# Performance work log

Measured on AMD Instinct MI355X. Metric: run time of the kernel, lower is better.

## Reference

```python
import jax, jax.numpy as jnp
import numpy as np

# 3x3 Hessian/derivative stencils (match torch tensors in edge_mask_deptehwise)
_DII = jnp.array([[0., 1., 0.], [0., -2., 0.], [0., 1., 0.]], jnp.float32).reshape(1, 1, 3, 3)
_DIJ = 0.25 * jnp.array([[1., 0., -1.], [0., 0., 0.], [-1., 0., 1.]], jnp.float32).reshape(1, 1, 3, 3)
_DJJ = jnp.array([[0., 0., 0.], [1., -2., 1.], [0., 0., 0.]], jnp.float32).reshape(1, 1, 3, 3)


def _conv3x3(x, kern):  # x: [1,1,h,w], zero padding 1 (matches F.conv2d padding=1)
    return jax.lax.conv_general_dilated(x, kern, (1, 1), ((1, 1), (1, 1)))


def _edge_mask(x, edge_thld):  # x: [1,1,h,w] -> bool [1,1,h,w]
    dii = _conv3x3(x, _DII)
    dij = _conv3x3(x, _DIJ)
    djj = _conv3x3(x, _DJJ)
    det = dii * djj - dij * dij
    tr = dii + djj
    thld = (edge_thld + 1) ** 2 / edge_thld
    return (tr * tr / det <= thld) & (det > 0)


def _max_pool(x, ksize):  # stride 1, padding 1 (matches F.max_pool2d(..., padding=1))
    return jax.lax.reduce_window(x, -jnp.inf, jax.lax.max,
                                 (1, 1, ksize, ksize), (1, 1, 1, 1),
                                 ((0, 0), (0, 0), (1, 1), (1, 1)))


def setup_inputs() -> dict:
    key = jax.random.key(0)
    k1, k2 = jax.random.split(key)
    h = w = 4096
    score_map = jax.random.uniform(k1, (1, 1, h, w), dtype=jnp.float32)
    valid_depth_mask = jax.random.randint(k2, (h, w), 0, 2).astype(jnp.bool_)
    return {
        'score_map': score_map,
        'valid_depth_mask': valid_depth_mask,
        'k': 4096,
        'score_thld': 0,
        'edge_thld': 10,
        'nms_size': 3,
        'eof_size': 5,
    }


def reference(score_map, valid_depth_mask, k, score_thld, edge_thld, nms_size, eof_size):
    b, c, h, w = score_map.shape  # b = c = 1 (extract_kpts reshapes to (h, w))
    mask = score_map > score_thld
    if nms_size > 0:
        nms_max = _max_pool(score_map, nms_size)
        mask = (score_map == nms_max) & mask
    if eof_size > 0:
        ri = jnp.arange(h)
        cj = jnp.arange(w)
        eof = ((ri >= eof_size) & (ri < h - eof_size))[:, None] & \
              ((cj >= eof_size) & (cj < w - eof_size))[None, :]
        mask = eof[None, None] & mask
    if edge_thld > 0:
        mask = _edge_mask(score_map, edge_thld) & mask
    mask2d = mask.reshape(h, w) & valid_depth_mask
    flat_scores = score_map.reshape(h * w)
    # nonzero + argsort(desc)[:k] + gather  ==  top_k over -inf-masked scores
    masked = jnp.where(mask2d.reshape(-1), flat_scores, -jnp.inf)
    _, idx = jax.lax.top_k(masked, k)
    rows = idx // w
    cols = idx % w
    indices = jnp.stack([rows, cols], axis=0)[None]  # [1, 2, k]
    scores = flat_scores[idx][None]                  # [1, k]
    return indices, scores
```

## Files before the change

kernel.cpp:

```cpp
#include <hip/hip_runtime.h>
#include <stdint.h>

#define H 4096
#define W 4096
#define EOFS 5
#define K_TOP 4096
#define NB 65536
#define SLOT_CAP 8192
#define RPB 16
#define CBUF 4096
#define EMIT_LDS (K_TOP + 128)


__device__ __forceinline__ unsigned int bucket_of(float s) {
    float u = s * s;
    float u2 = u * u;
    float u4 = u2 * u2;
    float s9 = u4 * s;
    unsigned int b = (unsigned int)(s9 * 65536.0f);
    return b > 65535u ? 65535u : b;
}

__global__ void zero_kernel(unsigned int* hist, unsigned int* pivot,
                            unsigned int* candCount) {
    int p = blockIdx.x * blockDim.x + threadIdx.x;
    if (p < NB) hist[p] = 0u;
    if (p == 0) { pivot[0] = 0u; candCount[0] = 0u; }
}

#define PROC(ta, tb, tc, td, te, tf, tg, th, ti, jj)                           \
    {                                                                          \
        int j = (jj);                                                          \
        if (j >= EOFS && j <= W - 1 - EOFS) {                                  \
            float e = (te);                                                    \
            if (e > 0.0f) {                                                    \
                float m = fmaxf(fmaxf(fmaxf((ta), (tb)), fmaxf((tc), (td))),   \
                                fmaxf(fmaxf((tf), (tg)), fmaxf((th), (ti))));  \
                if (e >= m) {                                                  \
                    float dii = ((tb) - 2.0f * e) + (th);                      \
                    float djj = ((td) - 2.0f * e) + (tf);                      \
                    float dij = 0.25f * ((((ta) - (tc)) - (tg)) + (ti));       \
                    float det = dii * djj - dij * dij;                         \
                    if (det > 0.0f) {                                          \
                        float tr = dii + djj;                                  \
                        if (tr * tr / det <= 12.1f) {                          \
                            if (vmask[(size_t)i * W + j] != 0) {               \
                                unsigned int fb = __float_as_uint(e);          \
                                atomicAdd(&hist[bucket_of(e)], 1u);            \
                                unsigned int pos = atomicAdd(&cnt, 1u);        \
                                if (pos < CBUF) {                              \
                                    unsigned int idx =                         \
                                        (unsigned int)i * W + (unsigned int)j; \
                                    buf[pos] =                                 \
                                        ((unsigned long long)fb << 32) |       \
                                        (unsigned int)(~idx);                  \
                                }                                              \
                            }                                                  \
                        }                                                      \
                    }                                                          \
                }                                                              \
            }                                                                  \
        }                                                                      \
    }

__global__ __launch_bounds__(1024)
void collect_kernel(const float* __restrict__ x, const int* __restrict__ vmask,
                    unsigned int* __restrict__ hist,
                    unsigned long long* __restrict__ cand,
                    unsigned int* __restrict__ candCount,
                    unsigned int cand_cap, int do_cand) {
    __shared__ unsigned long long buf[CBUF];
    __shared__ unsigned int cnt, gbase;
    int t = threadIdx.x;
    if (t == 0) cnt = 0u;
    __syncthreads();
    int j0 = t * 4;
    bool active = (t >= 1 && t <= 1022);
    int r0 = EOFS + (int)blockIdx.x * RPB;
    int rend = r0 + RPB - 1;
    if (rend > H - 1 - EOFS) rend = H - 1 - EOFS;

    float al, a0, a1, a2, a3, ar;
    float bl, b0, b1, b2, b3, br;
    float cl, c0, c1, c2, c3, cr;
    if (active) {
        { const float* p = x + (size_t)(r0 - 1) * W + j0; al = p[-1];
          float4 q = *(const float4*)p; a0 = q.x; a1 = q.y; a2 = q.z; a3 = q.w; ar = p[4]; }
        { const float* p = x + (size_t)r0 * W + j0; bl = p[-1];
          float4 q = *(const float4*)p; b0 = q.x; b1 = q.y; b2 = q.z; b3 = q.w; br = p[4]; }
    }
    for (int i = r0; i <= rend; ++i) {
        if (active) {
            { const float* p = x + (size_t)(i + 1) * W + j0; cl = p[-1];
              float4 q = *(const float4*)p; c0 = q.x; c1 = q.y; c2 = q.z; c3 = q.w; cr = p[4]; }
            PROC(al, a0, a1, bl, b0, b1, cl, c0, c1, j0 + 0);
            PROC(a0, a1, a2, b0, b1, b2, c0, c1, c2, j0 + 1);
            PROC(a1, a2, a3, b1, b2, b3, c1, c2, c3, j0 + 2);
            PROC(a2, a3, ar, b2, b3, br, c2, c3, cr, j0 + 3);
            al = bl; a0 = b0; a1 = b1; a2 = b2; a3 = b3; ar = br;
            bl = cl; b0 = c0; b1 = c1; b2 = c2; b3 = c3; br = cr;
        }
    }
    __syncthreads();
    if (do_cand) {
        unsigned int c = cnt;
        if (c > CBUF) c = CBUF;
        if (t == 0) gbase = atomicAdd(candCount, c);
        __syncthreads();
        unsigned int g0 = gbase;
        for (unsigned int p = t; p < c; p += 1024)
            if (g0 + p < cand_cap) cand[g0 + p] = buf[p];
    }
}

__global__ __launch_bounds__(64)
void coarse_kernel(const unsigned int* __restrict__ hist,
                   unsigned int* __restrict__ coarse) {
    int c = blockIdx.x, t = threadIdx.x;
    const unsigned int* h = hist + c * 256;
    unsigned int s = h[t] + h[t + 64] + h[t + 128] + h[t + 192];
    for (int off = 32; off > 0; off >>= 1) s += __shfl_down(s, off, 64);
    if (t == 0) coarse[c] = s;
}

__global__ __launch_bounds__(256)
void chunkscan_kernel(const unsigned int* __restrict__ coarse,
                      unsigned int* __restrict__ chunkExcl) {
    __shared__ unsigned int s[256];
    int t = threadIdx.x;
    unsigned int mine = coarse[t];
    s[t] = mine;
    __syncthreads();
    for (int off = 1; off < 256; off <<= 1) {
        unsigned int v = (t + off < 256) ? s[t + off] : 0u;
        __syncthreads();
        s[t] += v;
        __syncthreads();
    }
    chunkExcl[t] = s[t] - mine;
}

__global__ __launch_bounds__(256)
void basefill_kernel(const unsigned int* __restrict__ hist,
                     const unsigned int* __restrict__ chunkExcl,
                     unsigned int* __restrict__ base,
                     unsigned int* __restrict__ pivotOut) {
    __shared__ unsigned int s[256];
    int t = threadIdx.x;
    int b = blockIdx.x * 256 + t;
    unsigned int h = hist[b];
    s[t] = h;
    __syncthreads();
    for (int off = 1; off < 256; off <<= 1) {
        unsigned int v = (t + off < 256) ? s[t + off] : 0u;
        __syncthreads();
        s[t] += v;
        __syncthreads();
    }
    unsigned int bb = chunkExcl[blockIdx.x] + s[t] - h;
    base[b] = bb;
    if (bb < (unsigned int)K_TOP && bb + h >= (unsigned int)K_TOP)
        pivotOut[0] = (unsigned int)b;
}

__global__ __launch_bounds__(256)
void scatter_cand_kernel(const unsigned long long* __restrict__ cand,
                         const unsigned int* __restrict__ candCount,
                         const unsigned int* __restrict__ pivotPtr,
                         unsigned int* __restrict__ base,
                         unsigned long long* __restrict__ slots,
                         unsigned int cand_cap) {
    unsigned int n = *candCount;
    if (n > cand_cap) n = cand_cap;
    unsigned int pivot = *pivotPtr;
    unsigned int stride = gridDim.x * blockDim.x;
    for (unsigned int p = blockIdx.x * blockDim.x + threadIdx.x; p < n; p += stride) {
        unsigned long long k = cand[p];
        unsigned int fb = (unsigned int)(k >> 32);
        unsigned int bkt = bucket_of(__uint_as_float(fb));
        if (bkt >= pivot) {
            unsigned int pos = atomicAdd(&base[bkt], 1u);
            if (pos < (unsigned int)SLOT_CAP) slots[pos] = k;
        }
    }
}

__global__ void scatter_full_kernel(const float* __restrict__ x,
                                    const int* __restrict__ vmask,
                                    const unsigned int* __restrict__ pivotPtr,
                                    unsigned int* __restrict__ base,
                                    unsigned long long* __restrict__ slots) {
    int j = EOFS + blockIdx.x * blockDim.x + threadIdx.x;
    int i = EOFS + blockIdx.y;
    if (j > W - 1 - EOFS) return;
    const float* r0p = x + (size_t)(i - 1) * W + j;
    const float* r1p = x + (size_t)i * W + j;
    const float* r2p = x + (size_t)(i + 1) * W + j;
    float a = r0p[-1], b = r0p[0], c = r0p[1];
    float d = r1p[-1], e = r1p[0], f = r1p[1];
    float g = r2p[-1], h2 = r2p[0], i2 = r2p[1];
    if (!(e > 0.0f)) return;
    float m = fmaxf(fmaxf(fmaxf(a, b), fmaxf(c, d)),
                    fmaxf(fmaxf(f, g), fmaxf(h2, i2)));
    if (!(e >= m)) return;
    float dii = (b - 2.0f * e) + h2;
    float djj = (d - 2.0f * e) + f;
    float dij = 0.25f * (((a - c) - g) + i2);
    float det = dii * djj - dij * dij;
    if (!(det > 0.0f)) return;
    float tr = dii + djj;
    if (!(tr * tr / det <= 12.1f)) return;
    if (vmask[(size_t)i * W + j] == 0) return;
    unsigned int bkt = bucket_of(e);
    if (bkt >= pivotPtr[0]) {
        unsigned int pos = atomicAdd(&base[bkt], 1u);
        if (pos < (unsigned int)SLOT_CAP) {
            unsigned int idx = (unsigned int)i * W + (unsigned int)j;
            slots[pos] = ((unsigned long long)__float_as_uint(e) << 32)
                       | (unsigned int)(~idx);
        }
    }
}

__global__ __launch_bounds__(1024, 1)
void emit_kernel(const unsigned int* __restrict__ baseAfter,
                 const unsigned int* __restrict__ pivotPtr,
                 const unsigned long long* __restrict__ slots,
                 float* __restrict__ out) {
    __shared__ unsigned long long lds[EMIT_LDS];
    int t = threadIdx.x;
    for (int p = t; p < EMIT_LDS; p += 1024) lds[p] = slots[p];
    __syncthreads();
    unsigned int pivot = pivotPtr[0];
    for (int b = (int)pivot + t; b < NB; b += 1024) {
        unsigned int start = (b == 65535) ? 0u : baseAfter[b + 1];
        unsigned int end = baseAfter[b];
        if (end > (unsigned int)SLOT_CAP) end = (unsigned int)SLOT_CAP;
        if (end <= start || start >= (unsigned int)K_TOP) continue;
        unsigned int len = end - start;
        if (len > 128u) len = 128u;
        if (start + len > (unsigned int)EMIT_LDS) len = (unsigned int)EMIT_LDS - start;
        unsigned long long* a = &lds[start];
        for (unsigned int r = 1; r < len; ++r) {
            unsigned long long key = a[r];
            int q = (int)r - 1;
            while (q >= 0 && a[q] < key) { a[q + 1] = a[q]; --q; }
            a[q + 1] = key;
        }
        unsigned int emitN = len;
        if (start + emitN > (unsigned int)K_TOP) emitN = (unsigned int)K_TOP - start;
        for (unsigned int r = 0; r < emitN; ++r) {
            unsigned long long key = a[r];
            unsigned int fb = (unsigned int)(key >> 32);
            unsigned int idx = ~((unsigned int)key);
            unsigned int rank = start + r;
            out[rank]             = (float)(idx >> 12);
            out[K_TOP + rank]     = (float)(idx & (W - 1));
            out[2 * K_TOP + rank] = __uint_as_float(fb);
        }
    }
}

extern "C" void kernel_launch(void* const* d_in, const int* in_sizes, int n_in,
                              void* d_out, int out_size, void* d_ws, size_t ws_size,
                              hipStream_t stream) {
    const float* score = (const float*)d_in[0];
    const int* vmask = (const int*)d_in[1];
    unsigned char* ws = (unsigned char*)d_ws;
    unsigned int* hist      = (unsigned int*)ws;
    unsigned int* base      = (unsigned int*)(ws + 262144);
    unsigned int* coarse    = (unsigned int*)(ws + 524288);
    unsigned int* chunkExcl = (unsigned int*)(ws + 525312);
    unsigned int* pivot     = (unsigned int*)(ws + 526336);
    unsigned int* candCount = (unsigned int*)(ws + 526340);
    unsigned long long* slots = (unsigned long long*)(ws + 526848);
    unsigned long long* cand  = (unsigned long long*)(ws + 655360);
    float* out = (float*)d_out;

    unsigned int cand_cap = 0;
    int do_cand = 0;
    if (ws_size >= 655360ull + 8ull * 1000000ull) {
        size_t cap = (ws_size - 655360ull) / 8ull;
        if (cap > 2097152ull) cap = 2097152ull;
        cand_cap = (unsigned int)cap;
        do_cand = 1;
    }

    zero_kernel<<<NB / 1024, 1024, 0, stream>>>(hist, pivot, candCount);

    int nblk = (H - 2 * EOFS + RPB - 1) / RPB;
    collect_kernel<<<nblk, 1024, 0, stream>>>(score, vmask, hist, cand,
                                              candCount, cand_cap, do_cand);
    coarse_kernel<<<256, 64, 0, stream>>>(hist, coarse);
    chunkscan_kernel<<<1, 256, 0, stream>>>(coarse, chunkExcl);
    basefill_kernel<<<256, 256, 0, stream>>>(hist, chunkExcl, base, pivot);

    if (do_cand) {
        scatter_cand_kernel<<<512, 256, 0, stream>>>(cand, candCount, pivot,
                                                     base, slots, cand_cap);
    } else {
        dim3 blk(256, 1, 1), grd(16, H - 2 * EOFS, 1);
        scatter_full_kernel<<<grd, blk, 0, stream>>>(score, vmask, pivot, base, slots);
    }
    emit_kernel<<<1, 1024, 0, stream>>>(base, pivot, slots, out);
}
```

Before: 263.6 us.

## Process eight columns per thread with separable vertical max in collect kernel

Rewrites the candidate collection stencil so each thread handles eight consecutive columns, loaded with two float4 reads plus halo values. A per-column vertical max is computed once and reused across the three horizontal neighbours, replacing the full 8-way max for every pixel. The launch changes from 1024-thread blocks over 16 rows to 256-thread blocks over 8 rows, split into two column halves, which gives more blocks and smaller per-block candidate buffers. Halo loads at row edges now read the neighbouring row's elements instead of idling the edge threads. This is safe only because the border columns are excluded later by the EOF check.

```diff
diff --git a/kernel.cpp b/kernel.cpp
--- a/kernel.cpp
+++ b/kernel.cpp
@@ -7,8 +7,9 @@
 #define K_TOP 4096
 #define NB 65536
 #define SLOT_CAP 8192
-#define RPB 16
-#define CBUF 4096
+#define RPB 8
+#define CPT 8
+#define CBUF 2048
 #define EMIT_LDS (K_TOP + 128)
 
 
@@ -28,42 +29,18 @@
     if (p == 0) { pivot[0] = 0u; candCount[0] = 0u; }
 }
 
-#define PROC(ta, tb, tc, td, te, tf, tg, th, ti, jj)                           \
+#define LOADROW(arr, p)                                                        \
     {                                                                          \
-        int j = (jj);                                                          \
-        if (j >= EOFS && j <= W - 1 - EOFS) {                                  \
-            float e = (te);                                                    \
-            if (e > 0.0f) {                                                    \
-                float m = fmaxf(fmaxf(fmaxf((ta), (tb)), fmaxf((tc), (td))),   \
-                                fmaxf(fmaxf((tf), (tg)), fmaxf((th), (ti))));  \
-                if (e >= m) {                                                  \
-                    float dii = ((tb) - 2.0f * e) + (th);                      \
-                    float djj = ((td) - 2.0f * e) + (tf);                      \
-                    float dij = 0.25f * ((((ta) - (tc)) - (tg)) + (ti));       \
-                    float det = dii * djj - dij * dij;                         \
-                    if (det > 0.0f) {                                          \
-                        float tr = dii + djj;                                  \
-                        if (tr * tr / det <= 12.1f) {                          \
-                            if (vmask[(size_t)i * W + j] != 0) {               \
-                                unsigned int fb = __float_as_uint(e);          \
-                                atomicAdd(&hist[bucket_of(e)], 1u);            \
-                                unsigned int pos = atomicAdd(&cnt, 1u);        \
-                                if (pos < CBUF) {                              \
-                                    unsigned int idx =                         \
-                                        (unsigned int)i * W + (unsigned int)j; \
-                                    buf[pos] =                                 \
-                                        ((unsigned long long)fb << 32) |       \
-                                        (unsigned int)(~idx);                  \
-                                }                                              \
-                            }                                                  \
-                        }                                                      \
-                    }                                                          \
-                }                                                              \
-            }                                                                  \
-        }                                                                      \
-    }
-
-__global__ __launch_bounds__(1024)
+        const float* _p = (p);                                                 \
+        arr[0] = _p[-1];                                                       \
+        float4 _q0 = *(const float4*)_p;                                       \
+        float4 _q1 = *(const float4*)(_p + 4);                                 \
+        arr[1] = _q0.x; arr[2] = _q0.y; arr[3] = _q0.z; arr[4] = _q0.w;        \
+        arr[5] = _q1.x; arr[6] = _q1.y; arr[7] = _q1.z; arr[8] = _q1.w;        \
+        arr[9] = _p[8];                                                        \
+    }
+
+__global__ __launch_bounds__(256)
 void collect_kernel(const float* __restrict__ x, const int* __restrict__ vmask,
                     unsigned int* __restrict__ hist,
                     unsigned long long* __restrict__ cand,
@@ -74,33 +51,60 @@
     int t = threadIdx.x;
     if (t == 0) cnt = 0u;
     __syncthreads();
-    int j0 = t * 4;
-    bool active = (t >= 1 && t <= 1022);
-    int r0 = EOFS + (int)blockIdx.x * RPB;
+
+    int rowgroup = (int)blockIdx.x >> 1;
+    int cg = (int)blockIdx.x & 1;
+    int j0 = cg * 2048 + t * CPT;
+    int r0 = EOFS + rowgroup * RPB;
     int rend = r0 + RPB - 1;
     if (rend > H - 1 - EOFS) rend = H - 1 - EOFS;
 
-    float al, a0, a1, a2, a3, ar;
-    float bl, b0, b1, b2, b3, br;
-    float cl, c0, c1, c2, c3, cr;
-    if (active) {
-        { const float* p = x + (size_t)(r0 - 1) * W + j0; al = p[-1];
-          float4 q = *(const float4*)p; a0 = q.x; a1 = q.y; a2 = q.z; a3 = q.w; ar = p[4]; }
-        { const float* p = x + (size_t)r0 * W + j0; bl = p[-1];
-          float4 q = *(const float4*)p; b0 = q.x; b1 = q.y; b2 = q.z; b3 = q.w; br = p[4]; }
-    }
+    float A[10], B[10], C[10], vm[10];
+    LOADROW(A, x + (size_t)(r0 - 1) * W + j0);
+    LOADROW(B, x + (size_t)r0 * W + j0);
+
     for (int i = r0; i <= rend; ++i) {
-        if (active) {
-            { const float* p = x + (size_t)(i + 1) * W + j0; cl = p[-1];
-              float4 q = *(const float4*)p; c0 = q.x; c1 = q.y; c2 = q.z; c3 = q.w; cr = p[4]; }
-            PROC(al, a0, a1, bl, b0, b1, cl, c0, c1, j0 + 0);
-            PROC(a0, a1, a2, b0, b1, b2, c0, c1, c2, j0 + 1);
-            PROC(a1, a2, a3, b1, b2, b3, c1, c2, c3, j0 + 2);
-            PROC(a2, a3, ar, b2, b3, br, c2, c3, cr, j0 + 3);
-            al = bl; a0 = b0; a1 = b1; a2 = b2; a3 = b3; ar = br;
-            bl = cl; b0 = c0; b1 = c1; b2 = c2; b3 = c3; br = cr;
-        }
-    }
+        LOADROW(C, x + (size_t)(i + 1) * W + j0);
+        #pragma unroll
+        for (int c = 0; c < 10; ++c)
+            vm[c] = fmaxf(fmaxf(A[c], B[c]), C[c]);
+        #pragma unroll
+        for (int k = 1; k <= 8; ++k) {
+            int j = j0 + k - 1;
+            if (j >= EOFS && j <= W - 1 - EOFS) {
+                float e = B[k];
+                if (e > 0.0f) {
+                    float m = fmaxf(fmaxf(vm[k - 1], vm[k]), vm[k + 1]);
+                    if (e >= m) {
+                        float dii = (A[k] - 2.0f * e) + C[k];
+                        float djj = (B[k - 1] - 2.0f * e) + B[k + 1];
+                        float dij = 0.25f * (((A[k - 1] - A[k + 1]) - C[k - 1]) + C[k + 1]);
+                        float det = dii * djj - dij * dij;
+                        if (det > 0.0f) {
+                            float tr = dii + djj;
+                            if (tr * tr / det <= 12.1f) {
+                                if (vmask[(size_t)i * W + j] != 0) {
+                                    unsigned int fb = __float_as_uint(e);
+                                    atomicAdd(&hist[bucket_of(e)], 1u);
+                                    unsigned int pos = atomicAdd(&cnt, 1u);
+                                    if (pos < CBUF) {
+                                        unsigned int idx =
+                                            (unsigned int)i * W + (unsigned int)j;
+                                        buf[pos] =
+                                            ((unsigned long long)fb << 32) |
+                                            (unsigned int)(~idx);
+                                    }
+                                }
+                            }
+                        }
+                    }
+                }
+            }
+        }
+        #pragma unroll
+        for (int c = 0; c < 10; ++c) { A[c] = B[c]; B[c] = C[c]; }
+    }
+
     __syncthreads();
     if (do_cand) {
         unsigned int c = cnt;
@@ -108,7 +112,7 @@
         if (t == 0) gbase = atomicAdd(candCount, c);
         __syncthreads();
         unsigned int g0 = gbase;
-        for (unsigned int p = t; p < c; p += 1024)
+        for (unsigned int p = t; p < c; p += 256)
             if (g0 + p < cand_cap) cand[g0 + p] = buf[p];
     }
 }
@@ -288,9 +292,9 @@
 
     zero_kernel<<<NB / 1024, 1024, 0, stream>>>(hist, pivot, candCount);
 
-    int nblk = (H - 2 * EOFS + RPB - 1) / RPB;
-    collect_kernel<<<nblk, 1024, 0, stream>>>(score, vmask, hist, cand,
-                                              candCount, cand_cap, do_cand);
+    int rowgroups = (H - 2 * EOFS + RPB - 1) / RPB;
+    collect_kernel<<<rowgroups * 2, 256, 0, stream>>>(score, vmask, hist, cand,
+                                                      candCount, cand_cap, do_cand);
     coarse_kernel<<<256, 64, 0, stream>>>(hist, coarse);
     chunkscan_kernel<<<1, 256, 0, stream>>>(coarse, chunkExcl);
     basefill_kernel<<<256, 256, 0, stream>>>(hist, chunkExcl, base, pivot);
```

After: 254.4 us. 1.04x faster.
